# Kernel optimization log

Measured on AMD Instinct MI355X. Metric: run time of the kernel, lower is better.

## Reference

```python
import jax, jax.numpy as jnp
import numpy as np

N_NODES = 100000


def _gcn_conv(x, src, dst, W, b, n_nodes):
    # PyG GCNConv: out = D^{-1/2} (A + I) D^{-1/2} (x W) + b
    h = x @ W  # [N, out]
    # degree including self-loop
    ones = jnp.ones(src.shape[0], dtype=h.dtype)
    deg = jax.ops.segment_sum(ones, dst, num_segments=n_nodes) + 1.0
    dinv = jax.lax.rsqrt(deg)  # [N]
    # neighbor messages: gather from src, normalize, scatter-add to dst
    norm = dinv[src] * dinv[dst]  # [E]
    msg = h[src] * norm[:, None]  # [E, out]
    agg = jax.ops.segment_sum(msg, dst, num_segments=n_nodes)
    # self-loop contribution: norm_ii = dinv[i]^2
    agg = agg + h * (dinv * dinv)[:, None]
    return agg + b


def setup_inputs() -> dict:
    key = jax.random.key(0)
    ks = jax.random.split(key, 10)
    x = jax.random.normal(ks[0], (N_NODES, 64), dtype=jnp.float32)
    edge_index = jax.random.randint(ks[1], (2, 1000000), 0, N_NODES, dtype=jnp.int64)
    def glorot(k, shape):
        lim = np.sqrt(6.0 / (shape[0] + shape[1]))
        return jax.random.uniform(k, shape, jnp.float32, -lim, lim)
    return {
        "x": x,
        "edge_index": edge_index,
        "W1": glorot(ks[2], (64, 80)), "b1": jnp.zeros((80,), jnp.float32),
        "W2": glorot(ks[3], (80, 40)), "b2": jnp.zeros((40,), jnp.float32),
        "W3": glorot(ks[4], (40, 50)), "b3": jnp.zeros((50,), jnp.float32),
        "Wl": glorot(ks[5], (50, 10)), "bl": jnp.zeros((10,), jnp.float32),
    }


def reference(x, edge_index, W1, b1, W2, b2, W3, b3, Wl, bl):
    src, dst = edge_index[0], edge_index[1]
    n = x.shape[0]
    h = _gcn_conv(x, src, dst, W1, b1, n)
    h = jax.nn.leaky_relu(h, negative_slope=0.01)
    # dropout is identity in eval mode
    h = _gcn_conv(h, src, dst, W2, b2, n)
    h = jax.nn.leaky_relu(h, negative_slope=0.01)
    h = _gcn_conv(h, src, dst, W3, b3, n)
    h = jax.nn.leaky_relu(h, negative_slope=0.01)
    logits = h @ Wl + bl
    return jax.nn.log_softmax(logits, axis=1)
```

## Files before the change

kernel.cpp:

```cpp
#include <hip/hip_runtime.h>

#define LEAKY(v) ((v) > 0.0f ? (v) : 0.01f * (v))
#define NBUK_MAX 512

typedef __attribute__((ext_vector_type(8))) short bf16x8;
typedef __attribute__((ext_vector_type(4))) float f32x4;

__device__ __forceinline__ unsigned short f2bf(float f) {
    unsigned u = __float_as_uint(f);
    u += 0x7fffu + ((u >> 16) & 1u);
    return (unsigned short)(u >> 16);
}
__device__ __forceinline__ unsigned pack2bf(float lo, float hi) {
    return (unsigned)f2bf(lo) | ((unsigned)f2bf(hi) << 16);
}
__device__ __forceinline__ float4 bf4_to_f4(uint2 u) {
    float4 r;
    r.x = __uint_as_float(u.x << 16);
    r.y = __uint_as_float(u.x & 0xffff0000u);
    r.z = __uint_as_float(u.y << 16);
    r.w = __uint_as_float(u.y & 0xffff0000u);
    return r;
}

__device__ __forceinline__ int detect_is64(const unsigned* ei, int E) {
    __shared__ int is64_s;
    if (threadIdx.x == 0) {
        int z = 1;
        int limit = 2 * E < 128 ? 2 * E : 128;
        for (int i = 1; i < limit; i += 2)
            if (ei[i] != 0u) { z = 0; break; }
        is64_s = z;
    }
    __syncthreads();
    return is64_s;
}

__global__ __launch_bounds__(256) void bucket_count_kernel(
    const unsigned* __restrict__ ei, int* __restrict__ s32, int* __restrict__ d32,
    int* __restrict__ gcount, int E, int nblk, int nbuk, int ch) {
    __shared__ int hist[NBUK_MAX];
    int is64 = detect_is64(ei, E);
    for (int i = threadIdx.x; i < nbuk; i += 256) hist[i] = 0;
    __syncthreads();
    int base = blockIdx.x * ch;
    int lim = min(base + ch, E);
    for (int e = base + threadIdx.x; e < lim; e += 256) {
        int s, d;
        if (is64) {
            s = (int)ei[2 * (size_t)e];
            d = (int)ei[2 * (size_t)E + 2 * (size_t)e];
        } else {
            s = (int)ei[e];
            d = (int)ei[(size_t)E + e];
        }
        s32[e] = s;
        d32[e] = d;
        atomicAdd(&hist[d >> 8], 1);
    }
    __syncthreads();
    for (int i = threadIdx.x; i < nbuk; i += 256)
        gcount[(size_t)i * nblk + blockIdx.x] = hist[i];
}

__global__ __launch_bounds__(256) void bucket_total_kernel(
    const int* __restrict__ gcount, int* __restrict__ btot, int nblk) {
    __shared__ int s[256];
    int sum = 0;
    for (int i = threadIdx.x; i < nblk; i += 256)
        sum += gcount[(size_t)blockIdx.x * nblk + i];
    s[threadIdx.x] = sum;
    __syncthreads();
    for (int off = 128; off > 0; off >>= 1) {
        if (threadIdx.x < off) s[threadIdx.x] += s[threadIdx.x + off];
        __syncthreads();
    }
    if (threadIdx.x == 0) btot[blockIdx.x] = s[0];
}

__global__ __launch_bounds__(512) void scan_btot_kernel(
    const int* __restrict__ btot, int* __restrict__ bbase,
    int* __restrict__ row_ofs, int nbuk, int N, int E) {
    __shared__ int s[512];
    int t = threadIdx.x;
    int v = (t < nbuk) ? btot[t] : 0;
    s[t] = v;
    __syncthreads();
    for (int off = 1; off < 512; off <<= 1) {
        int add = (t >= off) ? s[t - off] : 0;
        __syncthreads();
        s[t] += add;
        __syncthreads();
    }
    if (t < nbuk) bbase[t] = s[t] - v;
    if (t == 0) { bbase[nbuk] = E; row_ofs[N] = E; }
}

__global__ __launch_bounds__(256) void scan_gcount_kernel(
    int* __restrict__ gcount, const int* __restrict__ bbase, int nblk) {
    __shared__ int s[256];
    int t = threadIdx.x;
    int v = (t < nblk) ? gcount[(size_t)blockIdx.x * nblk + t] : 0;
    s[t] = v;
    __syncthreads();
    for (int off = 1; off < 256; off <<= 1) {
        int add = (t >= off) ? s[t - off] : 0;
        __syncthreads();
        s[t] += add;
        __syncthreads();
    }
    if (t < nblk)
        gcount[(size_t)blockIdx.x * nblk + t] = bbase[blockIdx.x] + s[t] - v;
}

__global__ __launch_bounds__(256) void bucket_scatter_kernel(
    const int* __restrict__ s32, const int* __restrict__ d32,
    const int* __restrict__ gofs, unsigned* __restrict__ es_tmp,
    int E, int nblk, int nbuk, int ch) {
    __shared__ int cur[NBUK_MAX];
    for (int i = threadIdx.x; i < nbuk; i += 256)
        cur[i] = gofs[(size_t)i * nblk + blockIdx.x];
    __syncthreads();
    int base = blockIdx.x * ch;
    int lim = min(base + ch, E);
    for (int e = base + threadIdx.x; e < lim; e += 256) {
        int s = s32[e], d = d32[e];
        int p = atomicAdd(&cur[d >> 8], 1);
        es_tmp[p] = ((unsigned)(d & 255) << 24) | (unsigned)s;
    }
}

__global__ __launch_bounds__(256) void bucket_sortcvt_kernel(
    const unsigned* __restrict__ es_tmp, const int* __restrict__ bbase,
    int* __restrict__ es, int* __restrict__ row_ofs, float* __restrict__ dinv,
    const float* __restrict__ x, ushort4* __restrict__ xb, int N) {
    __shared__ int hist[256];
    __shared__ int lofs[256];
    __shared__ float sdinv[256];
    int b = blockIdx.x;
    int t = threadIdx.x;
    int beg = bbase[b], end = bbase[b + 1];
    hist[t] = 0;
    __syncthreads();
    for (int j = beg + t; j < end; j += 256)
        atomicAdd(&hist[es_tmp[j] >> 24], 1);
    __syncthreads();
    int v = hist[t];
    lofs[t] = v;
    __syncthreads();
    for (int off = 1; off < 256; off <<= 1) {
        int add = (t >= off) ? lofs[t - off] : 0;
        __syncthreads();
        lofs[t] += add;
        __syncthreads();
    }
    int excl = lofs[t] - v;
    int node = (b << 8) + t;
    float dv = rsqrtf((float)v + 1.0f);
    if (node <= N) row_ofs[node] = beg + excl;
    if (node < N) dinv[node] = dv;
    sdinv[t] = dv;
    __syncthreads();
    lofs[t] = beg + excl;
    __syncthreads();
    for (int j = beg + t; j < end; j += 256) {
        unsigned ed = es_tmp[j];
        int p = atomicAdd(&lofs[ed >> 24], 1);
        es[p] = (int)(ed & 0xFFFFFFu);
    }
    int qbase = (b << 8) * 16;
    for (int q = t; q < 256 * 16; q += 256) {
        int nl = q >> 4;
        int n = (b << 8) + nl;
        if (n >= N) break;
        float dn = sdinv[nl];
        float4 vv = ((const float4*)x)[qbase + q];
        ushort4 o;
        o.x = f2bf(vv.x * dn); o.y = f2bf(vv.y * dn);
        o.z = f2bf(vv.z * dn); o.w = f2bf(vv.w * dn);
        xb[qbase + q] = o;
    }
}

__global__ __launch_bounds__(256) void gather64_bf16_kernel(
    const unsigned short* __restrict__ hb, const int* __restrict__ es,
    const int* __restrict__ row_ofs, const float* __restrict__ dinv,
    unsigned short* __restrict__ agg, int N) {
    int wid = (blockIdx.x * blockDim.x + threadIdx.x) >> 6;
    int lane = threadIdx.x & 63;
    int g = lane >> 3, l = lane & 7;
    int node = wid * 8 + g;
    bool active = node < N;
    int beg = 0, end = 0;
    float dd = 0.f;
    if (active) {
        beg = row_ofs[node];
        end = row_ofs[node + 1];
        dd = dinv[node];
    }
    float4 aL = make_float4(0.f, 0.f, 0.f, 0.f);
    float4 aH = make_float4(0.f, 0.f, 0.f, 0.f);
    int j = beg;
    for (; j + 2 <= end; j += 2) {
        int s0 = es[j], s1 = es[j + 1];
        uint4 h0 = *(const uint4*)&hb[(size_t)s0 * 64 + 8 * l];
        uint4 h1 = *(const uint4*)&hb[(size_t)s1 * 64 + 8 * l];
        float4 l0 = bf4_to_f4(make_uint2(h0.x, h0.y));
        float4 i0 = bf4_to_f4(make_uint2(h0.z, h0.w));
        float4 l1 = bf4_to_f4(make_uint2(h1.x, h1.y));
        float4 i1 = bf4_to_f4(make_uint2(h1.z, h1.w));
        aL.x += l0.x + l1.x; aL.y += l0.y + l1.y;
        aL.z += l0.z + l1.z; aL.w += l0.w + l1.w;
        aH.x += i0.x + i1.x; aH.y += i0.y + i1.y;
        aH.z += i0.z + i1.z; aH.w += i0.w + i1.w;
    }
    if (j < end) {
        int s0 = es[j];
        uint4 h0 = *(const uint4*)&hb[(size_t)s0 * 64 + 8 * l];
        float4 l0 = bf4_to_f4(make_uint2(h0.x, h0.y));
        float4 i0 = bf4_to_f4(make_uint2(h0.z, h0.w));
        aL.x += l0.x; aL.y += l0.y; aL.z += l0.z; aL.w += l0.w;
        aH.x += i0.x; aH.y += i0.y; aH.z += i0.z; aH.w += i0.w;
    }
    if (active) {
        uint4 sr = *(const uint4*)&hb[(size_t)node * 64 + 8 * l];
        float4 sL = bf4_to_f4(make_uint2(sr.x, sr.y));
        float4 sH = bf4_to_f4(make_uint2(sr.z, sr.w));
        uint4 o;
        o.x = pack2bf((aL.x + sL.x) * dd, (aL.y + sL.y) * dd);
        o.y = pack2bf((aL.z + sL.z) * dd, (aL.w + sL.w) * dd);
        o.z = pack2bf((aH.x + sH.x) * dd, (aH.y + sH.y) * dd);
        o.w = pack2bf((aH.z + sH.z) * dd, (aH.w + sH.w) * dd);
        *(uint4*)&agg[(size_t)node * 64 + 8 * l] = o;
    }
}

template <bool BIAS, bool PRESCALE_LEAKY>
__global__ __launch_bounds__(256) void gather40_bf16_kernel(
    const unsigned short* __restrict__ hb, const int* __restrict__ es,
    const int* __restrict__ row_ofs, const float* __restrict__ dinv,
    const float* __restrict__ b, unsigned short* __restrict__ agg, int N) {
    int wid = (blockIdx.x * blockDim.x + threadIdx.x) >> 6;
    int lane = threadIdx.x & 63;
    int g = lane / 5;
    int l = lane - g * 5;
    int node = wid * 12 + g;
    bool active = (g < 12) && (node < N);
    int beg = 0, end = 0;
    float dd = 0.f;
    if (active) {
        beg = row_ofs[node];
        end = row_ofs[node + 1];
        dd = dinv[node];
    }
    float4 aL = make_float4(0.f, 0.f, 0.f, 0.f);
    float4 aH = make_float4(0.f, 0.f, 0.f, 0.f);
    int j = beg;
    for (; j + 2 <= end; j += 2) {
        int s0 = es[j], s1 = es[j + 1];
        uint4 h0 = *(const uint4*)&hb[(size_t)s0 * 40 + 8 * l];
        uint4 h1 = *(const uint4*)&hb[(size_t)s1 * 40 + 8 * l];
        float4 l0 = bf4_to_f4(make_uint2(h0.x, h0.y));
        float4 i0 = bf4_to_f4(make_uint2(h0.z, h0.w));
        float4 l1 = bf4_to_f4(make_uint2(h1.x, h1.y));
        float4 i1 = bf4_to_f4(make_uint2(h1.z, h1.w));
        aL.x += l0.x + l1.x; aL.y += l0.y + l1.y;
        aL.z += l0.z + l1.z; aL.w += l0.w + l1.w;
        aH.x += i0.x + i1.x; aH.y += i0.y + i1.y;
        aH.z += i0.z + i1.z; aH.w += i0.w + i1.w;
    }
    if (j < end) {
        int s0 = es[j];
        uint4 h0 = *(const uint4*)&hb[(size_t)s0 * 40 + 8 * l];
        float4 l0 = bf4_to_f4(make_uint2(h0.x, h0.y));
        float4 i0 = bf4_to_f4(make_uint2(h0.z, h0.w));
        aL.x += l0.x; aL.y += l0.y; aL.z += l0.z; aL.w += l0.w;
        aH.x += i0.x; aH.y += i0.y; aH.z += i0.z; aH.w += i0.w;
    }
    if (active) {
        uint4 sr = *(const uint4*)&hb[(size_t)node * 40 + 8 * l];
        float4 sL = bf4_to_f4(make_uint2(sr.x, sr.y));
        float4 sH = bf4_to_f4(make_uint2(sr.z, sr.w));
        float r0 = (aL.x + sL.x) * dd, r1 = (aL.y + sL.y) * dd;
        float r2 = (aL.z + sL.z) * dd, r3 = (aL.w + sL.w) * dd;
        float r4 = (aH.x + sH.x) * dd, r5 = (aH.y + sH.y) * dd;
        float r6 = (aH.z + sH.z) * dd, r7 = (aH.w + sH.w) * dd;
        if (BIAS) {
            float4 b0 = *(const float4*)&b[8 * l];
            float4 b1 = *(const float4*)&b[8 * l + 4];
            r0 += b0.x; r1 += b0.y; r2 += b0.z; r3 += b0.w;
            r4 += b1.x; r5 += b1.y; r6 += b1.z; r7 += b1.w;
        }
        if (PRESCALE_LEAKY) {
            r0 = LEAKY(r0) * dd; r1 = LEAKY(r1) * dd;
            r2 = LEAKY(r2) * dd; r3 = LEAKY(r3) * dd;
            r4 = LEAKY(r4) * dd; r5 = LEAKY(r5) * dd;
            r6 = LEAKY(r6) * dd; r7 = LEAKY(r7) * dd;
        }
        uint4 o;
        o.x = pack2bf(r0, r1); o.y = pack2bf(r2, r3);
        o.z = pack2bf(r4, r5); o.w = pack2bf(r6, r7);
        *(uint4*)&agg[(size_t)node * 40 + 8 * l] = o;
    }
}

__global__ __launch_bounds__(256) void prep_wfrags_kernel(
    const float* __restrict__ W1, const float* __restrict__ W2,
    unsigned short* __restrict__ wfrag) {
    int t = blockIdx.x * 256 + threadIdx.x;
    if (t >= 2432) return;
    const float* W;
    int u, NKC, M, K;
    if (t < 1280) { u = t; W = W1; NKC = 2; M = 80; K = 64; }
    else          { u = t - 1280; W = W2; NKC = 3; M = 40; K = 80; }
    int f = u >> 6, lane = u & 63;
    int s = f & 1, mtkc = f >> 1;
    int kc = mtkc % NKC, mt = mtkc / NKC;
    int col = mt * 16 + (lane & 15);
#pragma unroll
    for (int j = 0; j < 8; ++j) {
        int k = kc * 32 + ((lane >> 4) << 3) + j;
        float w = (k < K && col < M) ? W[k * M + col] : 0.0f;
        unsigned short hi = f2bf(w);
        unsigned short v = s ? f2bf(w - __uint_as_float((unsigned)hi << 16)) : hi;
        wfrag[(size_t)t * 8 + j] = v;
    }
}

template <int KBF, int M, int NKC, int NMT, bool LEAKY_OUT, bool BIAS, bool SCALE>
__global__ __launch_bounds__(256) void gemm_mfma_bf16(
    const unsigned short* __restrict__ X, const unsigned short* __restrict__ wfrag,
    const float* __restrict__ bvec, const float* __restrict__ dinv,
    unsigned short* __restrict__ out, int N) {
    static_assert(KBF <= NKC * 32 && M <= NMT * 16, "tile coverage");
    constexpr int NFR = NMT * NKC * 2;
    __shared__ bf16x8 wlds[NFR * 64];
    for (int i = threadIdx.x; i < NFR * 64; i += 256) {
        int f = i >> 6, ln = i & 63;
        wlds[f * 64 + (ln ^ (ln >> 3))] = *(const bf16x8*)&wfrag[(size_t)i * 8];
    }
    __syncthreads();
    int wid = blockIdx.x * 4 + (threadIdx.x >> 6);
    int ntiles = (N + 15) >> 4;
    if (wid >= ntiles) return;
    int lane = threadIdx.x & 63;
    int kid = lane >> 4;
    int lidx = lane ^ (lane >> 3);
    int base = wid * 16;
    int arow = base + (lane & 15);
    if (arow >= N) arow = N - 1;

    bf16x8 a[NKC];
#pragma unroll
    for (int kc = 0; kc < NKC; ++kc) {
        int k0 = kc * 32 + kid * 8;
        if (k0 < KBF)
            a[kc] = *(const bf16x8*)&X[(size_t)arow * KBF + k0];
        else
            a[kc] = (bf16x8){0, 0, 0, 0, 0, 0, 0, 0};
    }
    f32x4 acc[NMT];
#pragma unroll
    for (int mt = 0; mt < NMT; ++mt) acc[mt] = (f32x4){0.f, 0.f, 0.f, 0.f};
#pragma unroll
    for (int mt = 0; mt < NMT; ++mt) {
#pragma unroll
        for (int kc = 0; kc < NKC; ++kc) {
            acc[mt] = __builtin_amdgcn_mfma_f32_16x16x32_bf16(
                a[kc], wlds[((mt * NKC + kc) * 2 + 0) * 64 + lidx], acc[mt], 0, 0, 0);
            acc[mt] = __builtin_amdgcn_mfma_f32_16x16x32_bf16(
                a[kc], wlds[((mt * NKC + kc) * 2 + 1) * 64 + lidx], acc[mt], 0, 0, 0);
        }
    }
    float dv[4];
#pragma unroll
    for (int r = 0; r < 4; ++r)
        dv[r] = SCALE ? dinv[min(base + kid * 4 + r, N - 1)] : 1.0f;
#pragma unroll
    for (int mt = 0; mt < NMT; ++mt) {
        int col = mt * 16 + (lane & 15);
        if (col >= M) continue;
        float bb = BIAS ? bvec[col] : 0.0f;
#pragma unroll
        for (int r = 0; r < 4; ++r) {
            int orow = base + kid * 4 + r;
            if (orow < N) {
                float v = acc[mt][r] + bb;
                if (LEAKY_OUT) v = LEAKY(v);
                if (SCALE) v *= dv[r];
                out[(size_t)orow * M + col] = f2bf(v);
            }
        }
    }
}

__global__ __launch_bounds__(256) void l3head_kernel(
    const unsigned short* __restrict__ P, const float* __restrict__ W3,
    const float* __restrict__ b3, const float* __restrict__ Wl,
    const float* __restrict__ bl, float* __restrict__ out, int N) {
    __shared__ float w3s[40 * 50];
    __shared__ float b3s[50];
    __shared__ float wls[50 * 10];
    __shared__ float bls[10];
    for (int i = threadIdx.x; i < 2000; i += 256) w3s[i] = W3[i];
    for (int i = threadIdx.x; i < 500; i += 256) wls[i] = Wl[i];
    if (threadIdx.x < 50) b3s[threadIdx.x] = b3[threadIdx.x];
    if (threadIdx.x < 10) bls[threadIdx.x] = bl[threadIdx.x];
    __syncthreads();
    int n = blockIdx.x * blockDim.x + threadIdx.x;
    if (n >= N) return;

    float p[40];
    const uint2* pr = (const uint2*)(P + (size_t)n * 40);
#pragma unroll
    for (int q = 0; q < 10; ++q) {
        float4 t = bf4_to_f4(pr[q]);
        p[4 * q + 0] = t.x; p[4 * q + 1] = t.y; p[4 * q + 2] = t.z; p[4 * q + 3] = t.w;
    }
    float logits[10];
#pragma unroll
    for (int j = 0; j < 10; ++j) logits[j] = bls[j];
    for (int m = 0; m < 50; ++m) {
        float acc = b3s[m];
#pragma unroll
        for (int k = 0; k < 40; ++k) acc = fmaf(p[k], w3s[k * 50 + m], acc);
        float v = LEAKY(acc);
#pragma unroll
        for (int j = 0; j < 10; ++j) logits[j] = fmaf(v, wls[m * 10 + j], logits[j]);
    }
    float mx = logits[0];
#pragma unroll
    for (int j = 1; j < 10; ++j) mx = fmaxf(mx, logits[j]);
    float s = 0.0f;
#pragma unroll
    for (int j = 0; j < 10; ++j) s += __expf(logits[j] - mx);
    float lse = __logf(s) + mx;
    float* op = out + (size_t)n * 10;
#pragma unroll
    for (int j = 0; j < 10; ++j) op[j] = logits[j] - lse;
}

extern "C" void kernel_launch(void* const* d_in, const int* in_sizes, int n_in,
                              void* d_out, int out_size, void* d_ws, size_t ws_size,
                              hipStream_t stream) {
    const float* x  = (const float*)d_in[0];
    const unsigned* ei = (const unsigned*)d_in[1];
    const float* W1 = (const float*)d_in[2];
    const float* b1 = (const float*)d_in[3];
    const float* W2 = (const float*)d_in[4];
    const float* b2 = (const float*)d_in[5];
    const float* W3 = (const float*)d_in[6];
    const float* b3 = (const float*)d_in[7];
    const float* Wl = (const float*)d_in[8];
    const float* bl = (const float*)d_in[9];
    float* out = (float*)d_out;

    const int N = in_sizes[0] / 64;
    const int E = in_sizes[1] / 2;

    int ch = 4096;
    int nblk = (E + ch - 1) / ch;
    if (nblk > 256) { ch = (E + 255) / 256; nblk = (E + ch - 1) / ch; }
    const int nbuk = (N + 255) >> 8;

    char* wp = (char*)d_ws;
    auto alloc = [&](size_t bytes) {
        char* p = wp;
        wp += (bytes + 255) & ~(size_t)255;
        return p;
    };
    int*   es      = (int*)alloc((size_t)E * 4);
    float* dinv    = (float*)alloc((size_t)N * 4);
    int*   row_ofs = (int*)alloc((size_t)(N + 1) * 4);
    int*   gcount  = (int*)alloc((size_t)nbuk * nblk * 4);
    int*   btot    = (int*)alloc((size_t)NBUK_MAX * 4);
    int*   bbase   = (int*)alloc((size_t)(NBUK_MAX + 1) * 4);
    unsigned short* wfrag = (unsigned short*)alloc((size_t)2432 * 8 * 2);
    char*  Pr      = (char*)alloc((size_t)N * 64 * 4);
    char*  Ar      = (char*)alloc((size_t)N * 80 * 4);

    int*      s32    = (int*)Pr;
    int*      d32    = (int*)Pr + E;
    unsigned* es_tmp = (unsigned*)Ar;
    size_t xb_off = (((size_t)E * 4) + 255) & ~(size_t)255;
    unsigned short* xb = (unsigned short*)(Ar + xb_off);
    unsigned short* Pg = (unsigned short*)Pr;
    unsigned short* A  = (unsigned short*)Ar;
    unsigned short* Pb = (unsigned short*)Pr;
    unsigned short* Ab = (unsigned short*)(Ar + (size_t)N * 80 * 4 - (size_t)N * 40 * 2);
    unsigned short* P3 = (unsigned short*)Pr;

    const int B = 256;

    prep_wfrags_kernel<<<10, B, 0, stream>>>(W1, W2, wfrag);

    bucket_count_kernel<<<nblk, B, 0, stream>>>(ei, s32, d32, gcount, E, nblk, nbuk, ch);
    bucket_total_kernel<<<nbuk, B, 0, stream>>>(gcount, btot, nblk);
    scan_btot_kernel<<<1, 512, 0, stream>>>(btot, bbase, row_ofs, nbuk, N, E);
    scan_gcount_kernel<<<nbuk, B, 0, stream>>>(gcount, bbase, nblk);
    bucket_scatter_kernel<<<nblk, B, 0, stream>>>(s32, d32, gcount, es_tmp, E, nblk, nbuk, ch);
    bucket_sortcvt_kernel<<<nbuk, B, 0, stream>>>(es_tmp, bbase, es, row_ofs, dinv,
                                                  x, (ushort4*)xb, N);

    const int blk64 = ((N + 7) / 8 + 3) / 4;
    const int blk40 = ((N + 11) / 12 + 3) / 4;

    const int ntiles = (N + 15) / 16;
    const int gemm_blocks = (ntiles + 3) / 4;

    gather64_bf16_kernel<<<blk64, B, 0, stream>>>(xb, es, row_ofs, dinv, Pg, N);
    gemm_mfma_bf16<64, 80, 2, 5, true, true, false>
        <<<gemm_blocks, B, 0, stream>>>(Pg, wfrag, b1, nullptr, A, N);

    gemm_mfma_bf16<80, 40, 3, 3, false, false, true>
        <<<gemm_blocks, B, 0, stream>>>(A, wfrag + 20 * 512, nullptr, dinv, Pb, N);
    gather40_bf16_kernel<true, true><<<blk40, B, 0, stream>>>(Pb, es, row_ofs, dinv, b2, Ab, N);

    gather40_bf16_kernel<false, false><<<blk40, B, 0, stream>>>(Ab, es, row_ofs, dinv, nullptr, P3, N);
    l3head_kernel<<<(N + B - 1) / B, B, 0, stream>>>(P3, W3, b3, Wl, bl, out, N);
}
```

Baseline: 267.0 us.

## Fuse layer-1 neighbor gather into MFMA GEMM kernel and unroll gather40 by four

Layer-1 aggregation now runs inside the GEMM kernel. Each wave gathers the aggregated bf16 rows for 16 nodes directly into MFMA A-fragments (one node per row-lane group, 4 lanes per node) and multiplies them against the LDS-resident weight fragments. This removes the intermediate write and re-read of the N×64 aggregate and one kernel launch. The trade-off is fewer lanes per node in the gather (16 nodes per wave instead of 8 per 64 lanes, with two 16-byte loads per edge per lane), which may reduce memory-level parallelism. The gather40 edge loop is also unrolled from 2 to 4 edges to keep more loads in flight, and the buffer aliasing is adjusted.

```diff
diff --git a/kernel.cpp b/kernel.cpp
--- a/kernel.cpp
+++ b/kernel.cpp
@@ -182,56 +182,134 @@
     }
 }
 
-__global__ __launch_bounds__(256) void gather64_bf16_kernel(
-    const unsigned short* __restrict__ hb, const int* __restrict__ es,
+__global__ __launch_bounds__(256) void prep_wfrags_kernel(
+    const float* __restrict__ W1, const float* __restrict__ W2,
+    unsigned short* __restrict__ wfrag) {
+    int t = blockIdx.x * 256 + threadIdx.x;
+    if (t >= 2432) return;
+    const float* W;
+    int u, NKC, M, K;
+    if (t < 1280) { u = t; W = W1; NKC = 2; M = 80; K = 64; }
+    else          { u = t - 1280; W = W2; NKC = 3; M = 40; K = 80; }
+    int f = u >> 6, lane = u & 63;
+    int s = f & 1, mtkc = f >> 1;
+    int kc = mtkc % NKC, mt = mtkc / NKC;
+    int col = mt * 16 + (lane & 15);
+#pragma unroll
+    for (int j = 0; j < 8; ++j) {
+        int k = kc * 32 + ((lane >> 4) << 3) + j;
+        float w = (k < K && col < M) ? W[k * M + col] : 0.0f;
+        unsigned short hi = f2bf(w);
+        unsigned short v = s ? f2bf(w - __uint_as_float((unsigned)hi << 16)) : hi;
+        wfrag[(size_t)t * 8 + j] = v;
+    }
+}
+
+__global__ __launch_bounds__(256) void l1_fused_kernel(
+    const unsigned short* __restrict__ xb, const int* __restrict__ es,
     const int* __restrict__ row_ofs, const float* __restrict__ dinv,
-    unsigned short* __restrict__ agg, int N) {
-    int wid = (blockIdx.x * blockDim.x + threadIdx.x) >> 6;
+    const unsigned short* __restrict__ wfrag, const float* __restrict__ b1,
+    unsigned short* __restrict__ out, int N) {
+    constexpr int NFR = 20;
+    __shared__ bf16x8 wlds[NFR * 64];
+    for (int i = threadIdx.x; i < NFR * 64; i += 256) {
+        int f = i >> 6, ln = i & 63;
+        wlds[f * 64 + (ln ^ (ln >> 3))] = *(const bf16x8*)&wfrag[(size_t)i * 8];
+    }
+    __syncthreads();
+    int wid = blockIdx.x * 4 + (threadIdx.x >> 6);
+    int ntiles = (N + 15) >> 4;
+    if (wid >= ntiles) return;
     int lane = threadIdx.x & 63;
-    int g = lane >> 3, l = lane & 7;
-    int node = wid * 8 + g;
-    bool active = node < N;
+    int row = lane & 15, kid = lane >> 4;
+    int lidx = lane ^ (lane >> 3);
+    int base = wid * 16;
+    int node = base + row;
+    bool act = node < N;
     int beg = 0, end = 0;
     float dd = 0.f;
-    if (active) {
+    if (act) {
         beg = row_ofs[node];
         end = row_ofs[node + 1];
         dd = dinv[node];
     }
-    float4 aL = make_float4(0.f, 0.f, 0.f, 0.f);
-    float4 aH = make_float4(0.f, 0.f, 0.f, 0.f);
+    const char* xbb = (const char*)xb;
+    const int o0 = kid * 16;
+    const int o1 = 64 + kid * 16;
+    float4 aL0 = make_float4(0.f, 0.f, 0.f, 0.f);
+    float4 aL1 = make_float4(0.f, 0.f, 0.f, 0.f);
+    float4 aH0 = make_float4(0.f, 0.f, 0.f, 0.f);
+    float4 aH1 = make_float4(0.f, 0.f, 0.f, 0.f);
+#define ACCU(u, c0, c1)                                             \
+    {                                                               \
+        float4 lo_ = bf4_to_f4(make_uint2((u).x, (u).y));           \
+        float4 hi_ = bf4_to_f4(make_uint2((u).z, (u).w));           \
+        c0.x += lo_.x; c0.y += lo_.y; c0.z += lo_.z; c0.w += lo_.w; \
+        c1.x += hi_.x; c1.y += hi_.y; c1.z += hi_.z; c1.w += hi_.w; \
+    }
     int j = beg;
     for (; j + 2 <= end; j += 2) {
         int s0 = es[j], s1 = es[j + 1];
-        uint4 h0 = *(const uint4*)&hb[(size_t)s0 * 64 + 8 * l];
-        uint4 h1 = *(const uint4*)&hb[(size_t)s1 * 64 + 8 * l];
-        float4 l0 = bf4_to_f4(make_uint2(h0.x, h0.y));
-        float4 i0 = bf4_to_f4(make_uint2(h0.z, h0.w));
-        float4 l1 = bf4_to_f4(make_uint2(h1.x, h1.y));
-        float4 i1 = bf4_to_f4(make_uint2(h1.z, h1.w));
-        aL.x += l0.x + l1.x; aL.y += l0.y + l1.y;
-        aL.z += l0.z + l1.z; aL.w += l0.w + l1.w;
-        aH.x += i0.x + i1.x; aH.y += i0.y + i1.y;
-        aH.z += i0.z + i1.z; aH.w += i0.w + i1.w;
+        const char* p0 = xbb + (size_t)s0 * 128;
+        const char* p1 = xbb + (size_t)s1 * 128;
+        uint4 u00 = *(const uint4*)(p0 + o0);
+        uint4 u01 = *(const uint4*)(p0 + o1);
+        uint4 u10 = *(const uint4*)(p1 + o0);
+        uint4 u11 = *(const uint4*)(p1 + o1);
+        ACCU(u00, aL0, aL1) ACCU(u01, aH0, aH1)
+        ACCU(u10, aL0, aL1) ACCU(u11, aH0, aH1)
     }
     if (j < end) {
         int s0 = es[j];
-        uint4 h0 = *(const uint4*)&hb[(size_t)s0 * 64 + 8 * l];
-        float4 l0 = bf4_to_f4(make_uint2(h0.x, h0.y));
-        float4 i0 = bf4_to_f4(make_uint2(h0.z, h0.w));
-        aL.x += l0.x; aL.y += l0.y; aL.z += l0.z; aL.w += l0.w;
-        aH.x += i0.x; aH.y += i0.y; aH.z += i0.z; aH.w += i0.w;
-    }
-    if (active) {
-        uint4 sr = *(const uint4*)&hb[(size_t)node * 64 + 8 * l];
-        float4 sL = bf4_to_f4(make_uint2(sr.x, sr.y));
-        float4 sH = bf4_to_f4(make_uint2(sr.z, sr.w));
-        uint4 o;
-        o.x = pack2bf((aL.x + sL.x) * dd, (aL.y + sL.y) * dd);
-        o.y = pack2bf((aL.z + sL.z) * dd, (aL.w + sL.w) * dd);
-        o.z = pack2bf((aH.x + sH.x) * dd, (aH.y + sH.y) * dd);
-        o.w = pack2bf((aH.z + sH.z) * dd, (aH.w + sH.w) * dd);
-        *(uint4*)&agg[(size_t)node * 64 + 8 * l] = o;
+        const char* p0 = xbb + (size_t)s0 * 128;
+        uint4 u00 = *(const uint4*)(p0 + o0);
+        uint4 u01 = *(const uint4*)(p0 + o1);
+        ACCU(u00, aL0, aL1) ACCU(u01, aH0, aH1)
+    }
+    if (act) {
+        const char* ps = xbb + (size_t)node * 128;
+        uint4 us0 = *(const uint4*)(ps + o0);
+        uint4 us1 = *(const uint4*)(ps + o1);
+        ACCU(us0, aL0, aL1) ACCU(us1, aH0, aH1)
+    }
+#undef ACCU
+    bf16x8 a0, a1;
+    a0[0] = (short)f2bf(aL0.x * dd); a0[1] = (short)f2bf(aL0.y * dd);
+    a0[2] = (short)f2bf(aL0.z * dd); a0[3] = (short)f2bf(aL0.w * dd);
+    a0[4] = (short)f2bf(aL1.x * dd); a0[5] = (short)f2bf(aL1.y * dd);
+    a0[6] = (short)f2bf(aL1.z * dd); a0[7] = (short)f2bf(aL1.w * dd);
+    a1[0] = (short)f2bf(aH0.x * dd); a1[1] = (short)f2bf(aH0.y * dd);
+    a1[2] = (short)f2bf(aH0.z * dd); a1[3] = (short)f2bf(aH0.w * dd);
+    a1[4] = (short)f2bf(aH1.x * dd); a1[5] = (short)f2bf(aH1.y * dd);
+    a1[6] = (short)f2bf(aH1.z * dd); a1[7] = (short)f2bf(aH1.w * dd);
+
+    f32x4 acc[5];
+#pragma unroll
+    for (int mt = 0; mt < 5; ++mt) acc[mt] = (f32x4){0.f, 0.f, 0.f, 0.f};
+#pragma unroll
+    for (int mt = 0; mt < 5; ++mt) {
+        acc[mt] = __builtin_amdgcn_mfma_f32_16x16x32_bf16(
+            a0, wlds[((mt * 2 + 0) * 2 + 0) * 64 + lidx], acc[mt], 0, 0, 0);
+        acc[mt] = __builtin_amdgcn_mfma_f32_16x16x32_bf16(
+            a0, wlds[((mt * 2 + 0) * 2 + 1) * 64 + lidx], acc[mt], 0, 0, 0);
+        acc[mt] = __builtin_amdgcn_mfma_f32_16x16x32_bf16(
+            a1, wlds[((mt * 2 + 1) * 2 + 0) * 64 + lidx], acc[mt], 0, 0, 0);
+        acc[mt] = __builtin_amdgcn_mfma_f32_16x16x32_bf16(
+            a1, wlds[((mt * 2 + 1) * 2 + 1) * 64 + lidx], acc[mt], 0, 0, 0);
+    }
+#pragma unroll
+    for (int mt = 0; mt < 5; ++mt) {
+        int col = mt * 16 + (lane & 15);
+        float bb = b1[col];
+#pragma unroll
+        for (int r = 0; r < 4; ++r) {
+            int orow = base + kid * 4 + r;
+            if (orow < N) {
+                float v = acc[mt][r] + bb;
+                v = LEAKY(v);
+                out[(size_t)orow * 80 + col] = f2bf(v);
+            }
+        }
     }
 }
 
@@ -255,28 +333,28 @@
     }
     float4 aL = make_float4(0.f, 0.f, 0.f, 0.f);
     float4 aH = make_float4(0.f, 0.f, 0.f, 0.f);
+#define ACC40(u)                                                    \
+    {                                                               \
+        float4 lo_ = bf4_to_f4(make_uint2((u).x, (u).y));           \
+        float4 hi_ = bf4_to_f4(make_uint2((u).z, (u).w));           \
+        aL.x += lo_.x; aL.y += lo_.y; aL.z += lo_.z; aL.w += lo_.w; \
+        aH.x += hi_.x; aH.y += hi_.y; aH.z += hi_.z; aH.w += hi_.w; \
+    }
     int j = beg;
-    for (; j + 2 <= end; j += 2) {
-        int s0 = es[j], s1 = es[j + 1];
+    for (; j + 4 <= end; j += 4) {
+        int s0 = es[j], s1 = es[j + 1], s2 = es[j + 2], s3 = es[j + 3];
         uint4 h0 = *(const uint4*)&hb[(size_t)s0 * 40 + 8 * l];
         uint4 h1 = *(const uint4*)&hb[(size_t)s1 * 40 + 8 * l];
-        float4 l0 = bf4_to_f4(make_uint2(h0.x, h0.y));
-        float4 i0 = bf4_to_f4(make_uint2(h0.z, h0.w));
-        float4 l1 = bf4_to_f4(make_uint2(h1.x, h1.y));
-        float4 i1 = bf4_to_f4(make_uint2(h1.z, h1.w));
-        aL.x += l0.x + l1.x; aL.y += l0.y + l1.y;
-        aL.z += l0.z + l1.z; aL.w += l0.w + l1.w;
-        aH.x += i0.x + i1.x; aH.y += i0.y + i1.y;
-        aH.z += i0.z + i1.z; aH.w += i0.w + i1.w;
-    }
-    if (j < end) {
+        uint4 h2 = *(const uint4*)&hb[(size_t)s2 * 40 + 8 * l];
+        uint4 h3 = *(const uint4*)&hb[(size_t)s3 * 40 + 8 * l];
+        ACC40(h0) ACC40(h1) ACC40(h2) ACC40(h3)
+    }
+    for (; j < end; ++j) {
         int s0 = es[j];
         uint4 h0 = *(const uint4*)&hb[(size_t)s0 * 40 + 8 * l];
-        float4 l0 = bf4_to_f4(make_uint2(h0.x, h0.y));
-        float4 i0 = bf4_to_f4(make_uint2(h0.z, h0.w));
-        aL.x += l0.x; aL.y += l0.y; aL.z += l0.z; aL.w += l0.w;
-        aH.x += i0.x; aH.y += i0.y; aH.z += i0.z; aH.w += i0.w;
-    }
+        ACC40(h0)
+    }
+#undef ACC40
     if (active) {
         uint4 sr = *(const uint4*)&hb[(size_t)node * 40 + 8 * l];
         float4 sL = bf4_to_f4(make_uint2(sr.x, sr.y));
@@ -304,29 +382,6 @@
     }
 }
 
-__global__ __launch_bounds__(256) void prep_wfrags_kernel(
-    const float* __restrict__ W1, const float* __restrict__ W2,
-    unsigned short* __restrict__ wfrag) {
-    int t = blockIdx.x * 256 + threadIdx.x;
-    if (t >= 2432) return;
-    const float* W;
-    int u, NKC, M, K;
-    if (t < 1280) { u = t; W = W1; NKC = 2; M = 80; K = 64; }
-    else          { u = t - 1280; W = W2; NKC = 3; M = 40; K = 80; }
-    int f = u >> 6, lane = u & 63;
-    int s = f & 1, mtkc = f >> 1;
-    int kc = mtkc % NKC, mt = mtkc / NKC;
-    int col = mt * 16 + (lane & 15);
-#pragma unroll
-    for (int j = 0; j < 8; ++j) {
-        int k = kc * 32 + ((lane >> 4) << 3) + j;
-        float w = (k < K && col < M) ? W[k * M + col] : 0.0f;
-        unsigned short hi = f2bf(w);
-        unsigned short v = s ? f2bf(w - __uint_as_float((unsigned)hi << 16)) : hi;
-        wfrag[(size_t)t * 8 + j] = v;
-    }
-}
-
 template <int KBF, int M, int NKC, int NMT, bool LEAKY_OUT, bool BIAS, bool SCALE>
 __global__ __launch_bounds__(256) void gemm_mfma_bf16(
     const unsigned short* __restrict__ X, const unsigned short* __restrict__ wfrag,
@@ -484,9 +539,8 @@
     unsigned* es_tmp = (unsigned*)Ar;
     size_t xb_off = (((size_t)E * 4) + 255) & ~(size_t)255;
     unsigned short* xb = (unsigned short*)(Ar + xb_off);
-    unsigned short* Pg = (unsigned short*)Pr;
-    unsigned short* A  = (unsigned short*)Ar;
-    unsigned short* Pb = (unsigned short*)Pr;
+    unsigned short* A  = (unsigned short*)Pr;
+    unsigned short* Pb = (unsigned short*)Ar;
     unsigned short* Ab = (unsigned short*)(Ar + (size_t)N * 80 * 4 - (size_t)N * 40 * 2);
     unsigned short* P3 = (unsigned short*)Pr;
 
@@ -502,15 +556,11 @@
     bucket_sortcvt_kernel<<<nbuk, B, 0, stream>>>(es_tmp, bbase, es, row_ofs, dinv,
                                                   x, (ushort4*)xb, N);
 
-    const int blk64 = ((N + 7) / 8 + 3) / 4;
     const int blk40 = ((N + 11) / 12 + 3) / 4;
-
     const int ntiles = (N + 15) / 16;
     const int gemm_blocks = (ntiles + 3) / 4;
 
-    gather64_bf16_kernel<<<blk64, B, 0, stream>>>(xb, es, row_ofs, dinv, Pg, N);
-    gemm_mfma_bf16<64, 80, 2, 5, true, true, false>
-        <<<gemm_blocks, B, 0, stream>>>(Pg, wfrag, b1, nullptr, A, N);
+    l1_fused_kernel<<<gemm_blocks, B, 0, stream>>>(xb, es, row_ofs, dinv, wfrag, b1, A, N);
 
     gemm_mfma_bf16<80, 40, 3, 3, false, false, true>
         <<<gemm_blocks, B, 0, stream>>>(A, wfrag + 20 * 512, nullptr, dinv, Pb, N);
```

New measurement: 262.0 us. No clear change (-1.9%).
